# Optimization experiments

Hardware: AMD Instinct MI355X
Metric: run time of the kernel (lower is better)

Reference implementation:

```python
import jax, jax.numpy as jnp
import numpy as np

IN_F = 4096
OUT_F = 4096
BATCH = 256


def setup_inputs() -> dict:
    key = jax.random.key(0)
    ks = jax.random.split(key, 5)
    stdv = 1.0 / np.sqrt(IN_F)
    x = jax.random.normal(ks[0], (BATCH, IN_F), dtype=jnp.float32)
    weight_mu = jax.random.uniform(ks[1], (OUT_F, IN_F), dtype=jnp.float32, minval=-stdv, maxval=stdv)
    bias_mu = jax.random.uniform(ks[2], (OUT_F,), dtype=jnp.float32, minval=-stdv, maxval=stdv)
    weight_logvar = jnp.full((OUT_F, IN_F), -6.0, dtype=jnp.float32)
    bias_logvar = jnp.full((OUT_F,), -6.0, dtype=jnp.float32)
    weight_eps = jax.random.normal(ks[3], (OUT_F, IN_F), dtype=jnp.float32)
    bias_eps = jax.random.normal(ks[4], (OUT_F,), dtype=jnp.float32)
    return {
        "x": x,
        "weight_mu": weight_mu,
        "weight_logvar": weight_logvar,
        "bias_mu": bias_mu,
        "bias_logvar": bias_logvar,
        "weight_eps": weight_eps,
        "bias_eps": bias_eps,
    }


def reference(x, weight_mu, weight_logvar, bias_mu, bias_logvar, weight_eps, bias_eps):
    # Reparameterized sample: W = mu + eps * exp(0.5 * logvar)
    weight = weight_mu + weight_eps * jnp.exp(0.5 * weight_logvar)   # [O, I]
    bias = bias_mu + bias_eps * jnp.exp(0.5 * bias_logvar)           # [O]
    # F.linear: y = x @ W^T + b
    return jnp.einsum('bi,oi->bo', x, weight) + bias
```

## Files before the change

### kernel.cpp

```cpp
#include <hip/hip_runtime.h>
#include <stdint.h>
#include <stddef.h>

#define BATCH 256
#define IN_F  4096
#define OUT_F 4096
#define BN    16
#define BK    128
#define NT    (IN_F / BK)
#define TPB   512

#define RAW_BUF   24576
#define RAW_ARR   8192
#define BF_BASE   73728
#define LDS_TOTAL 81920

typedef __attribute__((ext_vector_type(8))) short    bf16x8;
typedef __attribute__((ext_vector_type(4))) float    f32x4;
typedef __attribute__((ext_vector_type(2))) uint32_t u32x2;
typedef __attribute__((ext_vector_type(4))) uint32_t u32x4;

#define MFMA(a,b,c) __builtin_amdgcn_mfma_f32_16x16x32_bf16((a),(b),(c),0,0,0)
#define HALF_LOG2E 0.7213475204444817f

__device__ __forceinline__ uint32_t pack2bf(float a, float b) {
  uint32_t ua = __builtin_bit_cast(uint32_t, a);
  uint32_t ub = __builtin_bit_cast(uint32_t, b);
  ua += 0x7FFFu + ((ua >> 16) & 1u);
  ub += 0x7FFFu + ((ub >> 16) & 1u);
  return (ua >> 16) | (ub & 0xFFFF0000u);
}

__device__ __forceinline__ bf16x8 cvt8(const float* p) {
  f32x4 v0 = *(const f32x4*)p;
  f32x4 v1 = *(const f32x4*)(p + 4);
  union { u32x4 u; bf16x8 h; } r;
  r.u[0] = pack2bf(v0[0], v0[1]); r.u[1] = pack2bf(v0[2], v0[3]);
  r.u[2] = pack2bf(v1[0], v1[1]); r.u[3] = pack2bf(v1[2], v1[3]);
  return r.h;
}

__device__ __forceinline__ void gload_lds16(const void* g, void* l) {
  __builtin_amdgcn_global_load_lds(
      (const __attribute__((address_space(1))) uint32_t*)g,
      (__attribute__((address_space(3))) uint32_t*)l, 16, 0, 0);
}

__global__ __launch_bounds__(256) void prep_kernel(
    const float* __restrict__ x,
    const float* __restrict__ bmu,
    const float* __restrict__ blv,
    const float* __restrict__ beps,
    u32x4* __restrict__ xs4,
    float* __restrict__ bias)
{
  const uint32_t b = blockIdx.x;
  if (b < 512u) {
    const uint32_t c = b * 256u + threadIdx.x;
    const float* p = x + (size_t)c * 8u;
    f32x4 v0 = *(const f32x4*)p;
    f32x4 v1 = *(const f32x4*)(p + 4);
    u32x4 o;
    o[0] = pack2bf(v0[0], v0[1]); o[1] = pack2bf(v0[2], v0[3]);
    o[2] = pack2bf(v1[0], v1[1]); o[3] = pack2bf(v1[2], v1[3]);
    xs4[c] = o;
  } else {
    const uint32_t i = (b - 512u) * 256u + threadIdx.x;
    bias[i] = fmaf(beps[i], exp2f(blv[i] * HALF_LOG2E), bmu[i]);
  }
}

template<bool USE_XS>
__global__ __launch_bounds__(TPB)
void vgemm(const uint16_t* __restrict__ xs,
           const float*    __restrict__ xf,
           const float*    __restrict__ wmu,
           const float*    __restrict__ wlv,
           const float*    __restrict__ weps,
           const float*    __restrict__ biasp,
           const float*    __restrict__ bmu,
           const float*    __restrict__ blv,
           const float*    __restrict__ beps,
           float*          __restrict__ y)
{
  __shared__ __align__(16) uint8_t lds[LDS_TOTAL];

  const int tid = threadIdx.x;
  const int wv  = tid >> 6;
  const int l   = tid & 63;
  const int n0  = blockIdx.x * BN;

  const int    sr   = tid >> 5;
  const size_t goff = (size_t)(n0 + sr) * IN_F + ((tid & 31) << 2);

  const int c16w = (tid & 31) >> 1;
  const int bfw  = sr * 256 + ((c16w ^ (sr & 7)) << 4) + ((tid & 1) << 3);

  const int br = l & 15;
  const int kb = l >> 4;
  const int bfo0 = br * 256 + (((0 * 4 + kb) ^ (br & 7)) << 4);
  const int bfo1 = br * 256 + (((1 * 4 + kb) ^ (br & 7)) << 4);
  const int bfo2 = br * 256 + (((2 * 4 + kb) ^ (br & 7)) << 4);
  const int bfo3 = br * 256 + (((3 * 4 + kb) ^ (br & 7)) << 4);
  const int arow0 = wv * 32 + br;

  f32x4 acc0 = {0.f, 0.f, 0.f, 0.f};
  f32x4 acc1 = {0.f, 0.f, 0.f, 0.f};

  auto STAGE = [&](int t, int buf) {
    const size_t go = goff + (size_t)t * BK;
    uint8_t* base = &lds[0] + buf * RAW_BUF + wv * 1024;
    gload_lds16(wmu  + go, base + 0 * RAW_ARR);
    gload_lds16(wlv  + go, base + 1 * RAW_ARR);
    gload_lds16(weps + go, base + 2 * RAW_ARR);
  };

  auto CVT = [&](int t) {
    const uint8_t* rb = &lds[0] + (t % 3) * RAW_BUF;
    f32x4 m = *(const f32x4*)(rb + 0 * RAW_ARR + tid * 16);
    f32x4 v = *(const f32x4*)(rb + 1 * RAW_ARR + tid * 16);
    f32x4 e = *(const f32x4*)(rb + 2 * RAW_ARR + tid * 16);
    u32x2 o;
    o[0] = pack2bf(fmaf(e[0], exp2f(v[0] * HALF_LOG2E), m[0]),
                   fmaf(e[1], exp2f(v[1] * HALF_LOG2E), m[1]));
    o[1] = pack2bf(fmaf(e[2], exp2f(v[2] * HALF_LOG2E), m[2]),
                   fmaf(e[3], exp2f(v[3] * HALF_LOG2E), m[3]));
    *(u32x2*)(&lds[0] + BF_BASE + (t & 1) * 4096 + bfw) = o;
  };

  auto COMP = [&](int t) {
    const uint8_t* bfb = &lds[0] + BF_BASE + (t & 1) * 4096;
    bf16x8 a00, a01, a02, a03, a10, a11, a12, a13;
    if constexpr (USE_XS) {
      const uint16_t* x0 = xs + (size_t)arow0 * IN_F + t * BK + kb * 8;
      const uint16_t* x1 = x0 + (size_t)16 * IN_F;
      a00 = *(const bf16x8*)(x0);      a01 = *(const bf16x8*)(x0 + 32);
      a02 = *(const bf16x8*)(x0 + 64); a03 = *(const bf16x8*)(x0 + 96);
      a10 = *(const bf16x8*)(x1);      a11 = *(const bf16x8*)(x1 + 32);
      a12 = *(const bf16x8*)(x1 + 64); a13 = *(const bf16x8*)(x1 + 96);
    } else {
      const float* x0 = xf + (size_t)arow0 * IN_F + t * BK + kb * 8;
      const float* x1 = x0 + (size_t)16 * IN_F;
      a00 = cvt8(x0);      a01 = cvt8(x0 + 32);
      a02 = cvt8(x0 + 64); a03 = cvt8(x0 + 96);
      a10 = cvt8(x1);      a11 = cvt8(x1 + 32);
      a12 = cvt8(x1 + 64); a13 = cvt8(x1 + 96);
    }
    bf16x8 b0 = *(const bf16x8*)(bfb + bfo0);
    bf16x8 b1 = *(const bf16x8*)(bfb + bfo1);
    bf16x8 b2 = *(const bf16x8*)(bfb + bfo2);
    bf16x8 b3 = *(const bf16x8*)(bfb + bfo3);
    acc0 = MFMA(a00, b0, acc0); acc1 = MFMA(a10, b0, acc1);
    acc0 = MFMA(a01, b1, acc0); acc1 = MFMA(a11, b1, acc1);
    acc0 = MFMA(a02, b2, acc0); acc1 = MFMA(a12, b2, acc1);
    acc0 = MFMA(a03, b3, acc0); acc1 = MFMA(a13, b3, acc1);
  };

  STAGE(0, 0);
  STAGE(1, 1);

  for (int t = 0; t < NT - 2; ++t) {
    STAGE(t + 2, (t + 2) % 3);
    asm volatile("s_waitcnt vmcnt(6)" ::: "memory");
    __builtin_amdgcn_s_barrier();
    CVT(t);
    asm volatile("s_waitcnt lgkmcnt(0)" ::: "memory");
    __builtin_amdgcn_s_barrier();
    COMP(t);
  }
  {
    asm volatile("s_waitcnt vmcnt(3)" ::: "memory");
    __builtin_amdgcn_s_barrier();
    CVT(NT - 2);
    asm volatile("s_waitcnt lgkmcnt(0)" ::: "memory");
    __builtin_amdgcn_s_barrier();
    COMP(NT - 2);
  }
  {
    asm volatile("s_waitcnt vmcnt(0)" ::: "memory");
    __builtin_amdgcn_s_barrier();
    CVT(NT - 1);
    asm volatile("s_waitcnt lgkmcnt(0)" ::: "memory");
    __builtin_amdgcn_s_barrier();
    COMP(NT - 1);
  }

  const int col = n0 + br;
  float bv;
  if constexpr (USE_XS) {
    bv = biasp[col];
  } else {
    bv = fmaf(beps[col], exp2f(blv[col] * HALF_LOG2E), bmu[col]);
  }
  const int rbase = wv * 32 + kb * 4;
#pragma unroll
  for (int i = 0; i < 4; ++i)
    y[(size_t)(rbase + i) * OUT_F + col] = acc0[i] + bv;
#pragma unroll
  for (int i = 0; i < 4; ++i)
    y[(size_t)(rbase + 16 + i) * OUT_F + col] = acc1[i] + bv;
}

extern "C" void kernel_launch(void* const* d_in, const int* in_sizes, int n_in,
                              void* d_out, int out_size, void* d_ws, size_t ws_size,
                              hipStream_t stream) {
  const float* x    = (const float*)d_in[0];
  const float* wmu  = (const float*)d_in[1];
  const float* wlv  = (const float*)d_in[2];
  const float* bmu  = (const float*)d_in[3];
  const float* blv  = (const float*)d_in[4];
  const float* beps = (const float*)d_in[5];
  const float* bepsB= (const float*)d_in[6];
  const float* weps = beps;
  const float* b_eps = bepsB;
  float* y = (float*)d_out;

  const size_t xs_bytes = (size_t)BATCH * IN_F * 2;
  const size_t need     = xs_bytes + (size_t)OUT_F * 4;

  if (d_ws != nullptr && ws_size >= need) {
    uint16_t* xsp  = (uint16_t*)d_ws;
    float*    bias = (float*)((char*)d_ws + xs_bytes);
    prep_kernel<<<528, 256, 0, stream>>>(x, bmu, blv, b_eps, (u32x4*)d_ws, bias);
    vgemm<true><<<OUT_F / BN, TPB, 0, stream>>>(
        xsp, nullptr, wmu, wlv, weps, bias, nullptr, nullptr, nullptr, y);
  } else {
    vgemm<false><<<OUT_F / BN, TPB, 0, stream>>>(
        nullptr, x, wmu, wlv, weps, nullptr, bmu, blv, b_eps, y);
  }
}
```

Measured before the change: 98.68 us.

## Split K across four blocks per column tile and add reduction kernel

Splits the K dimension four ways so there are four times as many blocks, each using 256 threads, a BK of 64 and a smaller LDS footprint, with a launch bound for multiple blocks per CU. Partial sums go to workspace and a separate reduce kernel adds them plus the bias. The aim is to fill more CUs and raise memory-level parallelism for streaming the three weight arrays. The cost is extra partial-sum traffic (four 4 MB buffers), one more kernel launch, and the loss of the three-stage pipeline with fine-grained waitcnt in favour of a simpler double buffer with full __syncthreads.

```diff
diff --git a/kernel.cpp b/kernel.cpp
--- a/kernel.cpp
+++ b/kernel.cpp
@@ -6,14 +6,14 @@
 #define IN_F  4096
 #define OUT_F 4096
 #define BN    16
-#define BK    128
-#define NT    (IN_F / BK)
-#define TPB   512
-
-#define RAW_BUF   24576
-#define RAW_ARR   8192
-#define BF_BASE   73728
-#define LDS_TOTAL 81920
+#define BK    64
+#define KSPLIT 4
+#define TPB   256
+
+#define RAW_BUF   12288
+#define RAW_ARR   4096
+#define BF_BASE   24576
+#define LDS_TOTAL 26624
 
 typedef __attribute__((ext_vector_type(8))) short    bf16x8;
 typedef __attribute__((ext_vector_type(4))) float    f32x4;
@@ -70,8 +70,8 @@
   }
 }
 
-template<bool USE_XS>
-__global__ __launch_bounds__(TPB)
+template<int NSPLIT, bool USE_XS>
+__global__ __launch_bounds__(TPB, 4)
 void vgemm(const uint16_t* __restrict__ xs,
            const float*    __restrict__ xf,
            const float*    __restrict__ wmu,
@@ -81,42 +81,43 @@
            const float*    __restrict__ bmu,
            const float*    __restrict__ blv,
            const float*    __restrict__ beps,
-           float*          __restrict__ y)
+           float*          __restrict__ out)
 {
   __shared__ __align__(16) uint8_t lds[LDS_TOTAL];
 
   const int tid = threadIdx.x;
   const int wv  = tid >> 6;
   const int l   = tid & 63;
-  const int n0  = blockIdx.x * BN;
-
-  const int    sr   = tid >> 5;
-  const size_t goff = (size_t)(n0 + sr) * IN_F + ((tid & 31) << 2);
-
-  const int c16w = (tid & 31) >> 1;
-  const int bfw  = sr * 256 + ((c16w ^ (sr & 7)) << 4) + ((tid & 1) << 3);
+  const int col_tile = blockIdx.x / NSPLIT;
+  const int ks       = blockIdx.x % NSPLIT;
+  const int n0  = col_tile * BN;
+  const int k0  = ks * (IN_F / NSPLIT);
+  const int NT  = (IN_F / NSPLIT) / BK;
+
+  const size_t sgoff = (size_t)(n0 + 4 * wv + (l >> 4)) * IN_F + k0 + ((l & 15) << 2);
+
+  const int cr = tid >> 4;
+  const int ci = tid & 15;
+  const int bfw = cr * 128 + ((((ci >> 1) ^ (cr & 7)) << 4)) + ((ci & 1) << 3);
 
   const int br = l & 15;
   const int kb = l >> 4;
-  const int bfo0 = br * 256 + (((0 * 4 + kb) ^ (br & 7)) << 4);
-  const int bfo1 = br * 256 + (((1 * 4 + kb) ^ (br & 7)) << 4);
-  const int bfo2 = br * 256 + (((2 * 4 + kb) ^ (br & 7)) << 4);
-  const int bfo3 = br * 256 + (((3 * 4 + kb) ^ (br & 7)) << 4);
-  const int arow0 = wv * 32 + br;
-
-  f32x4 acc0 = {0.f, 0.f, 0.f, 0.f};
-  f32x4 acc1 = {0.f, 0.f, 0.f, 0.f};
+  const int bfo0 = br * 128 + ((((0 * 4 + kb)) ^ (br & 7)) << 4);
+  const int bfo1 = br * 128 + ((((1 * 4 + kb)) ^ (br & 7)) << 4);
+  const int arow0 = wv * 64 + br;
+
+  f32x4 acc[4] = {{0,0,0,0},{0,0,0,0},{0,0,0,0},{0,0,0,0}};
 
   auto STAGE = [&](int t, int buf) {
-    const size_t go = goff + (size_t)t * BK;
+    const size_t go = sgoff + (size_t)t * BK;
     uint8_t* base = &lds[0] + buf * RAW_BUF + wv * 1024;
     gload_lds16(wmu  + go, base + 0 * RAW_ARR);
     gload_lds16(wlv  + go, base + 1 * RAW_ARR);
     gload_lds16(weps + go, base + 2 * RAW_ARR);
   };
 
-  auto CVT = [&](int t) {
-    const uint8_t* rb = &lds[0] + (t % 3) * RAW_BUF;
+  auto CVT = [&](int buf) {
+    const uint8_t* rb = &lds[0] + buf * RAW_BUF;
     f32x4 m = *(const f32x4*)(rb + 0 * RAW_ARR + tid * 16);
     f32x4 v = *(const f32x4*)(rb + 1 * RAW_ARR + tid * 16);
     f32x4 e = *(const f32x4*)(rb + 2 * RAW_ARR + tid * 16);
@@ -125,80 +126,76 @@
                    fmaf(e[1], exp2f(v[1] * HALF_LOG2E), m[1]));
     o[1] = pack2bf(fmaf(e[2], exp2f(v[2] * HALF_LOG2E), m[2]),
                    fmaf(e[3], exp2f(v[3] * HALF_LOG2E), m[3]));
-    *(u32x2*)(&lds[0] + BF_BASE + (t & 1) * 4096 + bfw) = o;
+    *(u32x2*)(&lds[0] + BF_BASE + bfw) = o;
   };
 
   auto COMP = [&](int t) {
-    const uint8_t* bfb = &lds[0] + BF_BASE + (t & 1) * 4096;
-    bf16x8 a00, a01, a02, a03, a10, a11, a12, a13;
-    if constexpr (USE_XS) {
-      const uint16_t* x0 = xs + (size_t)arow0 * IN_F + t * BK + kb * 8;
-      const uint16_t* x1 = x0 + (size_t)16 * IN_F;
-      a00 = *(const bf16x8*)(x0);      a01 = *(const bf16x8*)(x0 + 32);
-      a02 = *(const bf16x8*)(x0 + 64); a03 = *(const bf16x8*)(x0 + 96);
-      a10 = *(const bf16x8*)(x1);      a11 = *(const bf16x8*)(x1 + 32);
-      a12 = *(const bf16x8*)(x1 + 64); a13 = *(const bf16x8*)(x1 + 96);
-    } else {
-      const float* x0 = xf + (size_t)arow0 * IN_F + t * BK + kb * 8;
-      const float* x1 = x0 + (size_t)16 * IN_F;
-      a00 = cvt8(x0);      a01 = cvt8(x0 + 32);
-      a02 = cvt8(x0 + 64); a03 = cvt8(x0 + 96);
-      a10 = cvt8(x1);      a11 = cvt8(x1 + 32);
-      a12 = cvt8(x1 + 64); a13 = cvt8(x1 + 96);
-    }
+    const uint8_t* bfb = &lds[0] + BF_BASE;
     bf16x8 b0 = *(const bf16x8*)(bfb + bfo0);
     bf16x8 b1 = *(const bf16x8*)(bfb + bfo1);
-    bf16x8 b2 = *(const bf16x8*)(bfb + bfo2);
-    bf16x8 b3 = *(const bf16x8*)(bfb + bfo3);
-    acc0 = MFMA(a00, b0, acc0); acc1 = MFMA(a10, b0, acc1);
-    acc0 = MFMA(a01, b1, acc0); acc1 = MFMA(a11, b1, acc1);
-    acc0 = MFMA(a02, b2, acc0); acc1 = MFMA(a12, b2, acc1);
-    acc0 = MFMA(a03, b3, acc0); acc1 = MFMA(a13, b3, acc1);
+    const size_t kb0 = (size_t)k0 + t * BK + kb * 8;
+#pragma unroll
+    for (int j = 0; j < 4; ++j) {
+      bf16x8 a0, a1;
+      if constexpr (USE_XS) {
+        const uint16_t* xp = xs + (size_t)(arow0 + 16 * j) * IN_F + kb0;
+        a0 = *(const bf16x8*)(xp);
+        a1 = *(const bf16x8*)(xp + 32);
+      } else {
+        const float* xp = xf + (size_t)(arow0 + 16 * j) * IN_F + kb0;
+        a0 = cvt8(xp);
+        a1 = cvt8(xp + 32);
+      }
+      acc[j] = MFMA(a0, b0, acc[j]);
+      acc[j] = MFMA(a1, b1, acc[j]);
+    }
   };
 
   STAGE(0, 0);
-  STAGE(1, 1);
-
-  for (int t = 0; t < NT - 2; ++t) {
-    STAGE(t + 2, (t + 2) % 3);
-    asm volatile("s_waitcnt vmcnt(6)" ::: "memory");
-    __builtin_amdgcn_s_barrier();
-    CVT(t);
-    asm volatile("s_waitcnt lgkmcnt(0)" ::: "memory");
-    __builtin_amdgcn_s_barrier();
+  for (int t = 0; t < NT; ++t) {
+    if (t + 1 < NT) STAGE(t + 1, (t + 1) & 1);
+    __syncthreads();
+    CVT(t & 1);
+    __syncthreads();
     COMP(t);
   }
-  {
-    asm volatile("s_waitcnt vmcnt(3)" ::: "memory");
-    __builtin_amdgcn_s_barrier();
-    CVT(NT - 2);
-    asm volatile("s_waitcnt lgkmcnt(0)" ::: "memory");
-    __builtin_amdgcn_s_barrier();
-    COMP(NT - 2);
-  }
-  {
-    asm volatile("s_waitcnt vmcnt(0)" ::: "memory");
-    __builtin_amdgcn_s_barrier();
-    CVT(NT - 1);
-    asm volatile("s_waitcnt lgkmcnt(0)" ::: "memory");
-    __builtin_amdgcn_s_barrier();
-    COMP(NT - 1);
-  }
 
   const int col = n0 + br;
-  float bv;
-  if constexpr (USE_XS) {
-    bv = biasp[col];
+  if constexpr (NSPLIT == 1) {
+    float bv;
+    if constexpr (USE_XS) bv = biasp[col];
+    else bv = fmaf(beps[col], exp2f(blv[col] * HALF_LOG2E), bmu[col]);
+#pragma unroll
+    for (int j = 0; j < 4; ++j) {
+      const int rbase = wv * 64 + j * 16 + kb * 4;
+#pragma unroll
+      for (int i = 0; i < 4; ++i)
+        out[(size_t)(rbase + i) * OUT_F + col] = acc[j][i] + bv;
+    }
   } else {
-    bv = fmaf(beps[col], exp2f(blv[col] * HALF_LOG2E), bmu[col]);
-  }
-  const int rbase = wv * 32 + kb * 4;
-#pragma unroll
-  for (int i = 0; i < 4; ++i)
-    y[(size_t)(rbase + i) * OUT_F + col] = acc0[i] + bv;
-#pragma unroll
-  for (int i = 0; i < 4; ++i)
-    y[(size_t)(rbase + 16 + i) * OUT_F + col] = acc1[i] + bv;
+    float* po = out + (size_t)ks * BATCH * OUT_F;
+#pragma unroll
+    for (int j = 0; j < 4; ++j) {
+      const int rbase = wv * 64 + j * 16 + kb * 4;
+#pragma unroll
+      for (int i = 0; i < 4; ++i)
+        po[(size_t)(rbase + i) * OUT_F + col] = acc[j][i];
+    }
+  }
+}
+
+__global__ __launch_bounds__(256) void reduce_kernel(
+    const float* __restrict__ parts,
+    const float* __restrict__ bias,
+    float* __restrict__ y)
+{
+  const size_t e = ((size_t)blockIdx.x * 256 + threadIdx.x) * 4;
+  f32x4 s = *(const f32x4*)(parts + e);
+#pragma unroll
+  for (int p = 1; p < KSPLIT; ++p)
+    s += *(const f32x4*)(parts + (size_t)p * BATCH * OUT_F + e);
+  s += *(const f32x4*)(bias + (e & (OUT_F - 1)));
+  *(f32x4*)(y + e) = s;
 }
 
 extern "C" void kernel_launch(void* const* d_in, const int* in_sizes, int n_in,
@@ -209,23 +206,30 @@
   const float* wlv  = (const float*)d_in[2];
   const float* bmu  = (const float*)d_in[3];
   const float* blv  = (const float*)d_in[4];
-  const float* beps = (const float*)d_in[5];
-  const float* bepsB= (const float*)d_in[6];
-  const float* weps = beps;
-  const float* b_eps = bepsB;
+  const float* weps = (const float*)d_in[5];
+  const float* beps = (const float*)d_in[6];
   float* y = (float*)d_out;
 
-  const size_t xs_bytes = (size_t)BATCH * IN_F * 2;
-  const size_t need     = xs_bytes + (size_t)OUT_F * 4;
-
-  if (d_ws != nullptr && ws_size >= need) {
+  const size_t xs_b   = (size_t)BATCH * IN_F * 2;
+  const size_t bias_b = (size_t)OUT_F * 4;
+  const size_t part_b = (size_t)KSPLIT * BATCH * OUT_F * 4;
+
+  if (d_ws != nullptr && ws_size >= xs_b + bias_b + part_b) {
+    uint16_t* xsp   = (uint16_t*)d_ws;
+    float*    bias  = (float*)((char*)d_ws + xs_b);
+    float*    parts = (float*)((char*)d_ws + xs_b + bias_b);
+    prep_kernel<<<528, 256, 0, stream>>>(x, bmu, blv, beps, (u32x4*)d_ws, bias);
+    vgemm<KSPLIT, true><<<(OUT_F / BN) * KSPLIT, TPB, 0, stream>>>(
+        xsp, nullptr, wmu, wlv, weps, bias, nullptr, nullptr, nullptr, parts);
+    reduce_kernel<<<(BATCH * OUT_F) / (256 * 4), 256, 0, stream>>>(parts, bias, y);
+  } else if (d_ws != nullptr && ws_size >= xs_b + bias_b) {
     uint16_t* xsp  = (uint16_t*)d_ws;
-    float*    bias = (float*)((char*)d_ws + xs_bytes);
-    prep_kernel<<<528, 256, 0, stream>>>(x, bmu, blv, b_eps, (u32x4*)d_ws, bias);
-    vgemm<true><<<OUT_F / BN, TPB, 0, stream>>>(
+    float*    bias = (float*)((char*)d_ws + xs_b);
+    prep_kernel<<<528, 256, 0, stream>>>(x, bmu, blv, beps, (u32x4*)d_ws, bias);
+    vgemm<1, true><<<OUT_F / BN, TPB, 0, stream>>>(
         xsp, nullptr, wmu, wlv, weps, bias, nullptr, nullptr, nullptr, y);
   } else {
-    vgemm<false><<<OUT_F / BN, TPB, 0, stream>>>(
-        nullptr, x, wmu, wlv, weps, nullptr, bmu, blv, b_eps, y);
-  }
-}
+    vgemm<1, false><<<OUT_F / BN, TPB, 0, stream>>>(
+        nullptr, x, wmu, wlv, weps, nullptr, bmu, blv, beps, y);
+  }
+}
```

Measured after the change: 83.29 us. -15.6%, faster.
